# Optimization experiments

Measured on AMD Instinct MI355X. Metric: run time of the kernel, lower is better.

## Reference

```python
import jax, jax.numpy as jnp
import numpy as np

FP8_MAX = 448.0  # float8_e4m3fn max representable magnitude


def _fp8_quant_dequant(x, axis=-1):
    # Per-token (last-axis) dynamic scaling to e4m3, then dequantize back.
    scale = jnp.max(jnp.abs(x), axis=axis, keepdims=True) / FP8_MAX
    scale = jnp.maximum(scale, 1e-12)
    q = (x / scale).astype(jnp.float8_e4m3fn).astype(jnp.float32)
    return q * scale


def setup_inputs() -> dict:
    key = jax.random.key(0)
    k1, k2, k3, k4 = jax.random.split(key, 4)
    S, H, D, T = 64, 64, 128, 32768
    index_q = jax.random.normal(k1, (S, H, D), dtype=jnp.float32)
    index_k = jax.random.normal(k2, (T, D), dtype=jnp.float32)
    weights = jax.random.uniform(k3, (S, H), dtype=jnp.float32)
    cu_seqlen_ks = jnp.zeros((S,), dtype=jnp.int32)
    cu_seqlen_ke = jax.random.randint(k4, (S,), 1, T + 1, dtype=jnp.int32)
    return {
        "index_q": index_q,
        "index_k": index_k,
        "weights": weights,
        "cu_seqlen_ks": cu_seqlen_ks,
        "cu_seqlen_ke": cu_seqlen_ke,
    }


def reference(index_q, index_k, weights, cu_seqlen_ks, cu_seqlen_ke):
    # FP8 (e4m3) quantize-dequantize with per-token dynamic scales.
    q = _fp8_quant_dequant(index_q, axis=-1)   # [S, H, D]
    k = _fp8_quant_dequant(index_k, axis=-1)   # [T, D]
    # Index scores: relu(q.k) weighted-summed over heads -> [S, T]
    scores = jax.nn.relu(jnp.einsum("shd,td->sht", q, k))
    logits = jnp.einsum("sht,sh->st", scores, weights)
    # Ragged KV masking: query s sees kv tokens in [ks[s], ke[s]).
    t = jnp.arange(k.shape[0], dtype=jnp.int32)
    mask = (t[None, :] >= cu_seqlen_ks[:, None]) & (t[None, :] < cu_seqlen_ke[:, None])
    return jnp.where(mask, logits, -jnp.inf)
```

## Files before the change

### kernel.cpp

```cpp
#include <hip/hip_runtime.h>
#include <stdint.h>
#include <math.h>

#define NS 64
#define NH 64
#define ND 128
#define NT 32768
#define CH 1024

#define MASK_VAL (-3.0e38f)

typedef __attribute__((ext_vector_type(4))) float f32x4;

__device__ __align__(16) uint8_t g_q8[NS * NH * ND];
__device__ __align__(16) uint8_t g_k8[NT * ND];
__device__ __align__(16) float g_wq[NS * NH];
__device__ __align__(16) float g_sk[NT];

__device__ __forceinline__ uint32_t f32_to_e4m3(float x) {
  uint32_t u = __float_as_uint(x);
  uint32_t sign = (u >> 24) & 0x80u;
  uint32_t a = u & 0x7FFFFFFFu;
  if (a > 0x43E00000u) a = 0x43E00000u;
  uint32_t e = a >> 23;
  uint32_t code;
  if (e >= 121u) {
    uint32_t m = a & 0x7FFFFFu;
    m += 0x7FFFFu + ((m >> 20) & 1u);
    uint32_t carry = m >> 23;
    code = ((e - 120u + carry) << 3) | (carry ? 0u : ((m >> 20) & 7u));
    if (code > 0x7Eu) code = 0x7Eu;
  } else {
    code = (uint32_t)(int)rintf(__uint_as_float(a) * 512.0f);
  }
  return sign | code;
}

__device__ __forceinline__ void quant_frag(
    const float* __restrict__ in, uint8_t* __restrict__ q8out,
    float* __restrict__ scale_out, const float* __restrict__ wmul,
    int row, int o) {
  const float4* rp = reinterpret_cast<const float4*>(in) + (size_t)row * 32;
  float4 v0 = rp[o * 2];
  float4 v1 = rp[o * 2 + 1];
  float m = fmaxf(fmaxf(fmaxf(fabsf(v0.x), fabsf(v0.y)),
                        fmaxf(fabsf(v0.z), fabsf(v0.w))),
                  fmaxf(fmaxf(fabsf(v1.x), fabsf(v1.y)),
                        fmaxf(fabsf(v1.z), fabsf(v1.w))));
#pragma unroll
  for (int off = 8; off >= 1; off >>= 1)
    m = fmaxf(m, __shfl_xor(m, off, 64));
  float scale = fmaxf(m / 448.0f, 1e-12f);
  uint64_t q = 0;
  q |= (uint64_t)f32_to_e4m3(v0.x / scale);
  q |= (uint64_t)f32_to_e4m3(v0.y / scale) << 8;
  q |= (uint64_t)f32_to_e4m3(v0.z / scale) << 16;
  q |= (uint64_t)f32_to_e4m3(v0.w / scale) << 24;
  q |= (uint64_t)f32_to_e4m3(v1.x / scale) << 32;
  q |= (uint64_t)f32_to_e4m3(v1.y / scale) << 40;
  q |= (uint64_t)f32_to_e4m3(v1.z / scale) << 48;
  q |= (uint64_t)f32_to_e4m3(v1.w / scale) << 56;
  *reinterpret_cast<uint64_t*>(
      q8out + ((size_t)(row >> 4)) * 2048 + o * 128 + (row & 15) * 8) = q;
  if (o == 0) scale_out[row] = wmul ? wmul[row] * scale : scale;
}

__global__ __launch_bounds__(256) void quant_q_kernel(
    const float* __restrict__ in, const float* __restrict__ weights) {
  int w = threadIdx.x >> 6, l = threadIdx.x & 63;
  quant_frag(in, g_q8, g_wq, weights,
             blockIdx.x * 16 + w * 4 + (l >> 4), l & 15);
}

__global__ __launch_bounds__(256) void quant_k_kernel(
    const float* __restrict__ in) {
  int w = threadIdx.x >> 6, l = threadIdx.x & 63;
  quant_frag(in, g_k8, g_sk, nullptr,
             blockIdx.x * 16 + w * 4 + (l >> 4), l & 15);
}

__global__ __launch_bounds__(256) void indexer_main_kernel(
    const int* __restrict__ ksA, const int* __restrict__ keA,
    float* __restrict__ out) {
  const int s = blockIdx.x;
  const int c0 = blockIdx.y * CH;
  const int ks = ksA[s], ke = keA[s];
  const int tid = threadIdx.x;
  float* orow = out + (size_t)s * NT;

  if (c0 >= ke || c0 + CH <= ks) {
#pragma unroll
    for (int i = 0; i < CH / 256; ++i)
      orow[c0 + i * 256 + tid] = MASK_VAL;
    return;
  }

  const int l = tid & 63;
  const int w = tid >> 6;
  const int col = l & 15;
  const int g = l >> 4;

  long a[4][4];
#pragma unroll
  for (int kc = 0; kc < 4; ++kc)
#pragma unroll
    for (int ht = 0; ht < 4; ++ht)
      a[kc][ht] = *reinterpret_cast<const long*>(
          g_q8 + ((size_t)(s * 4 + ht)) * 2048 + kc * 512 + l * 8);

  float4 wq4[4];
#pragma unroll
  for (int ht = 0; ht < 4; ++ht)
    wq4[ht] = *reinterpret_cast<const float4*>(g_wq + s * NH + ht * 16 + g * 4);

#pragma unroll
  for (int i = 0; i < CH / 256; ++i) {
    const int t0w = c0 + i * 256 + w * 64;
    const int t = t0w + l;
    if (t0w >= ke || t0w + 64 <= ks) {
      orow[t] = MASK_VAL;
      continue;
    }

    f32x4 acc[4][4];
    const f32x4 z = {0.f, 0.f, 0.f, 0.f};
#pragma unroll
    for (int x = 0; x < 4; ++x)
#pragma unroll
      for (int y = 0; y < 4; ++y) acc[x][y] = z;

    const uint8_t* kbase = g_k8 + ((size_t)(t0w >> 4)) * 2048;
#pragma unroll
    for (int kc = 0; kc < 4; ++kc) {
      long b[4];
#pragma unroll
      for (int tt = 0; tt < 4; ++tt)
        b[tt] = *reinterpret_cast<const long*>(
            kbase + tt * 2048 + kc * 512 + l * 8);
#pragma unroll
      for (int ht = 0; ht < 4; ++ht)
#pragma unroll
        for (int tt = 0; tt < 4; ++tt)
          acc[ht][tt] = __builtin_amdgcn_mfma_f32_16x16x32_fp8_fp8(
              a[kc][ht], b[tt], acc[ht][tt], 0, 0, 0);
    }

    float r[4];
#pragma unroll
    for (int tt = 0; tt < 4; ++tt) {
      float p = 0.f;
#pragma unroll
      for (int ht = 0; ht < 4; ++ht) {
        p += wq4[ht].x * fmaxf(acc[ht][tt][0], 0.f);
        p += wq4[ht].y * fmaxf(acc[ht][tt][1], 0.f);
        p += wq4[ht].z * fmaxf(acc[ht][tt][2], 0.f);
        p += wq4[ht].w * fmaxf(acc[ht][tt][3], 0.f);
      }
      p += __shfl_xor(p, 16, 64);
      p += __shfl_xor(p, 32, 64);
      r[tt] = p;
    }
    float val = (g == 0) ? r[0] : (g == 1) ? r[1] : (g == 2) ? r[2] : r[3];
    val *= g_sk[t];
    if (((__float_as_uint(val) >> 23) & 0xFFu) == 0xFFu) val = 0.0f;
    orow[t] = (t >= ks && t < ke) ? val : MASK_VAL;
  }
}

extern "C" void kernel_launch(void* const* d_in, const int* in_sizes, int n_in,
                              void* d_out, int out_size, void* d_ws, size_t ws_size,
                              hipStream_t stream) {
  (void)in_sizes; (void)n_in; (void)out_size; (void)d_ws; (void)ws_size;
  const float* index_q = (const float*)d_in[0];
  const float* index_k = (const float*)d_in[1];
  const float* weights = (const float*)d_in[2];
  const int* ksA = (const int*)d_in[3];
  const int* keA = (const int*)d_in[4];
  float* out = (float*)d_out;

  quant_q_kernel<<<dim3((NS * NH) / 16), 256, 0, stream>>>(index_q, weights);
  quant_k_kernel<<<dim3(NT / 16), 256, 0, stream>>>(index_k);
  indexer_main_kernel<<<dim3(NS, NT / CH), 256, 0, stream>>>(ksA, keA, out);
}
```

Measured before the change: 48.83 us.

## Double-buffer K fragment loads across strips and raise occupancy hint

The main kernel now loads each strip's full set of K fragments into one of two register buffers ahead of time, prefetching the next strip while the MFMAs of the current strip run. The aim is to hide global-load latency that was previously exposed before each strip's MFMA chain. Launch bounds also request at least two blocks per CU, which caps register use, while the extra buffered registers add pressure and could cause spills. Prefetch loads are issued even for strips that end up masked, which adds some wasted bandwidth.

```diff
diff --git a/kernel.cpp b/kernel.cpp
--- a/kernel.cpp
+++ b/kernel.cpp
@@ -79,7 +79,60 @@
              blockIdx.x * 16 + w * 4 + (l >> 4), l & 15);
 }
 
-__global__ __launch_bounds__(256) void indexer_main_kernel(
+#define LOADB(BUF, I) do {                                                  \
+    const uint8_t* kb_ = g_k8 + (size_t)(c0 + (I) * 256 + w * 64) * 128;    \
+    _Pragma("unroll")                                                       \
+    for (int kc_ = 0; kc_ < 4; ++kc_)                                       \
+      _Pragma("unroll")                                                     \
+      for (int tt_ = 0; tt_ < 4; ++tt_)                                     \
+        BUF[kc_][tt_] = *reinterpret_cast<const long*>(                     \
+            kb_ + tt_ * 2048 + kc_ * 512 + l * 8);                          \
+  } while (0)
+
+#define STRIP(BUF, I) do {                                                  \
+    const int t0w_ = c0 + (I) * 256 + w * 64;                               \
+    const int t_ = t0w_ + l;                                                \
+    if (t0w_ >= ke || t0w_ + 64 <= ks) {                                    \
+      orow[t_] = MASK_VAL;                                                  \
+    } else {                                                                \
+      f32x4 acc[4][4];                                                      \
+      const f32x4 z_ = {0.f, 0.f, 0.f, 0.f};                                \
+      _Pragma("unroll")                                                     \
+      for (int x_ = 0; x_ < 4; ++x_)                                        \
+        _Pragma("unroll")                                                   \
+        for (int y_ = 0; y_ < 4; ++y_) acc[x_][y_] = z_;                    \
+      _Pragma("unroll")                                                     \
+      for (int kc_ = 0; kc_ < 4; ++kc_)                                     \
+        _Pragma("unroll")                                                   \
+        for (int ht_ = 0; ht_ < 4; ++ht_)                                   \
+          _Pragma("unroll")                                                 \
+          for (int tt_ = 0; tt_ < 4; ++tt_)                                 \
+            acc[ht_][tt_] = __builtin_amdgcn_mfma_f32_16x16x32_fp8_fp8(     \
+                a[kc_][ht_], BUF[kc_][tt_], acc[ht_][tt_], 0, 0, 0);        \
+      float r_[4];                                                          \
+      _Pragma("unroll")                                                     \
+      for (int tt_ = 0; tt_ < 4; ++tt_) {                                   \
+        float p_ = 0.f;                                                     \
+        _Pragma("unroll")                                                   \
+        for (int ht_ = 0; ht_ < 4; ++ht_) {                                 \
+          p_ += wq4[ht_].x * fmaxf(acc[ht_][tt_][0], 0.f);                  \
+          p_ += wq4[ht_].y * fmaxf(acc[ht_][tt_][1], 0.f);                  \
+          p_ += wq4[ht_].z * fmaxf(acc[ht_][tt_][2], 0.f);                  \
+          p_ += wq4[ht_].w * fmaxf(acc[ht_][tt_][3], 0.f);                  \
+        }                                                                   \
+        p_ += __shfl_xor(p_, 16, 64);                                       \
+        p_ += __shfl_xor(p_, 32, 64);                                       \
+        r_[tt_] = p_;                                                       \
+      }                                                                     \
+      float val_ = (g == 0) ? r_[0] : (g == 1) ? r_[1]                      \
+                 : (g == 2) ? r_[2] : r_[3];                                \
+      val_ *= g_sk[t_];                                                     \
+      if (((__float_as_uint(val_) >> 23) & 0xFFu) == 0xFFu) val_ = 0.0f;    \
+      orow[t_] = (t_ >= ks && t_ < ke) ? val_ : MASK_VAL;                   \
+    }                                                                       \
+  } while (0)
+
+__global__ __launch_bounds__(256, 2) void indexer_main_kernel(
     const int* __restrict__ ksA, const int* __restrict__ keA,
     float* __restrict__ out) {
   const int s = blockIdx.x;
@@ -99,6 +152,7 @@
   const int w = tid >> 6;
   const int col = l & 15;
   const int g = l >> 4;
+  (void)col;
 
   long a[4][4];
 #pragma unroll
@@ -113,58 +167,15 @@
   for (int ht = 0; ht < 4; ++ht)
     wq4[ht] = *reinterpret_cast<const float4*>(g_wq + s * NH + ht * 16 + g * 4);
 
-#pragma unroll
-  for (int i = 0; i < CH / 256; ++i) {
-    const int t0w = c0 + i * 256 + w * 64;
-    const int t = t0w + l;
-    if (t0w >= ke || t0w + 64 <= ks) {
-      orow[t] = MASK_VAL;
-      continue;
-    }
-
-    f32x4 acc[4][4];
-    const f32x4 z = {0.f, 0.f, 0.f, 0.f};
-#pragma unroll
-    for (int x = 0; x < 4; ++x)
-#pragma unroll
-      for (int y = 0; y < 4; ++y) acc[x][y] = z;
-
-    const uint8_t* kbase = g_k8 + ((size_t)(t0w >> 4)) * 2048;
-#pragma unroll
-    for (int kc = 0; kc < 4; ++kc) {
-      long b[4];
-#pragma unroll
-      for (int tt = 0; tt < 4; ++tt)
-        b[tt] = *reinterpret_cast<const long*>(
-            kbase + tt * 2048 + kc * 512 + l * 8);
-#pragma unroll
-      for (int ht = 0; ht < 4; ++ht)
-#pragma unroll
-        for (int tt = 0; tt < 4; ++tt)
-          acc[ht][tt] = __builtin_amdgcn_mfma_f32_16x16x32_fp8_fp8(
-              a[kc][ht], b[tt], acc[ht][tt], 0, 0, 0);
-    }
-
-    float r[4];
-#pragma unroll
-    for (int tt = 0; tt < 4; ++tt) {
-      float p = 0.f;
-#pragma unroll
-      for (int ht = 0; ht < 4; ++ht) {
-        p += wq4[ht].x * fmaxf(acc[ht][tt][0], 0.f);
-        p += wq4[ht].y * fmaxf(acc[ht][tt][1], 0.f);
-        p += wq4[ht].z * fmaxf(acc[ht][tt][2], 0.f);
-        p += wq4[ht].w * fmaxf(acc[ht][tt][3], 0.f);
-      }
-      p += __shfl_xor(p, 16, 64);
-      p += __shfl_xor(p, 32, 64);
-      r[tt] = p;
-    }
-    float val = (g == 0) ? r[0] : (g == 1) ? r[1] : (g == 2) ? r[2] : r[3];
-    val *= g_sk[t];
-    if (((__float_as_uint(val) >> 23) & 0xFFu) == 0xFFu) val = 0.0f;
-    orow[t] = (t >= ks && t < ke) ? val : MASK_VAL;
-  }
+  long bP[4][4], bQ[4][4];
+  LOADB(bP, 0);
+  LOADB(bQ, 1);
+  STRIP(bP, 0);
+  LOADB(bP, 2);
+  STRIP(bQ, 1);
+  LOADB(bQ, 3);
+  STRIP(bP, 2);
+  STRIP(bQ, 3);
 }
 
 extern "C" void kernel_launch(void* const* d_in, const int* in_sizes, int n_in,
```

After: 48.05 us. No clear change (-1.6%).

## Pair ke-sorted queries per block to reuse K fragments across two rows

Applied to the files above, without the earlier changes.

Adds a tiny kernel that sorts query rows by their ke end index, then has each main-kernel block process two adjacent sorted queries for one 1024-token chunk. The block loads the K fp8 fragments once and reuses them for both queries' MFMA passes. This halves K reads and gives paired rows similar masking extents, so fewer warps idle. The cost is an extra kernel launch, a dependency on the sort, higher register pressure with both Q fragment sets, and launch bounds of 2 blocks per CU.

```diff
diff --git a/kernel.cpp b/kernel.cpp
--- a/kernel.cpp
+++ b/kernel.cpp
@@ -7,6 +7,8 @@
 #define ND 128
 #define NT 32768
 #define CH 1024
+#define NCH (NT / CH)
+#define SB 2
 
 #define MASK_VAL (-3.0e38f)
 
@@ -16,6 +18,7 @@
 __device__ __align__(16) uint8_t g_k8[NT * ND];
 __device__ __align__(16) float g_wq[NS * NH];
 __device__ __align__(16) float g_sk[NT];
+__device__ int g_perm[NS];
 
 __device__ __forceinline__ uint32_t f32_to_e4m3(float x) {
   uint32_t u = __float_as_uint(x);
@@ -79,91 +82,127 @@
              blockIdx.x * 16 + w * 4 + (l >> 4), l & 15);
 }
 
-__global__ __launch_bounds__(256) void indexer_main_kernel(
+__global__ void sort_ke_kernel(const int* __restrict__ keA) {
+  int l = threadIdx.x;
+  int ke = keA[l];
+  int rank = 0;
+#pragma unroll
+  for (int o = 0; o < NS; ++o) {
+    int keo = __shfl(ke, o, 64);
+    rank += (keo > ke) || (keo == ke && o < l);
+  }
+  g_perm[rank] = l;
+}
+
+__global__ __launch_bounds__(256, 2) void indexer_main_kernel(
     const int* __restrict__ ksA, const int* __restrict__ keA,
     float* __restrict__ out) {
-  const int s = blockIdx.x;
-  const int c0 = blockIdx.y * CH;
-  const int ks = ksA[s], ke = keA[s];
+  const int c0 = blockIdx.x * CH;
+  const int sg = blockIdx.y;
   const int tid = threadIdx.x;
-  float* orow = out + (size_t)s * NT;
-
-  if (c0 >= ke || c0 + CH <= ks) {
-#pragma unroll
-    for (int i = 0; i < CH / 256; ++i)
-      orow[c0 + i * 256 + tid] = MASK_VAL;
-    return;
-  }
-
   const int l = tid & 63;
   const int w = tid >> 6;
-  const int col = l & 15;
   const int g = l >> 4;
 
-  long a[4][4];
+  const int s0 = g_perm[sg * 2], s1 = g_perm[sg * 2 + 1];
+  const int ks0 = ksA[s0], ke0 = keA[s0];
+  const int ks1 = ksA[s1], ke1 = keA[s1];
+  float* orow0 = out + (size_t)s0 * NT;
+  float* orow1 = out + (size_t)s1 * NT;
+
+  const bool act0 = (c0 < ke0) && (c0 + CH > ks0);
+  const bool act1 = (c0 < ke1) && (c0 + CH > ks1);
+  if (!act0 && !act1) {
+#pragma unroll
+    for (int i = 0; i < CH / 256; ++i) {
+      orow0[c0 + i * 256 + tid] = MASK_VAL;
+      orow1[c0 + i * 256 + tid] = MASK_VAL;
+    }
+    return;
+  }
+
+  long a0[4][4], a1[4][4];
 #pragma unroll
   for (int kc = 0; kc < 4; ++kc)
 #pragma unroll
-    for (int ht = 0; ht < 4; ++ht)
-      a[kc][ht] = *reinterpret_cast<const long*>(
-          g_q8 + ((size_t)(s * 4 + ht)) * 2048 + kc * 512 + l * 8);
-
-  float4 wq4[4];
-#pragma unroll
-  for (int ht = 0; ht < 4; ++ht)
-    wq4[ht] = *reinterpret_cast<const float4*>(g_wq + s * NH + ht * 16 + g * 4);
-
-#pragma unroll
-  for (int i = 0; i < CH / 256; ++i) {
+    for (int ht = 0; ht < 4; ++ht) {
+      a0[kc][ht] = *reinterpret_cast<const long*>(
+          g_q8 + ((size_t)(s0 * 4 + ht)) * 2048 + kc * 512 + l * 8);
+      a1[kc][ht] = *reinterpret_cast<const long*>(
+          g_q8 + ((size_t)(s1 * 4 + ht)) * 2048 + kc * 512 + l * 8);
+    }
+  float4 w0[4], w1[4];
+#pragma unroll
+  for (int ht = 0; ht < 4; ++ht) {
+    w0[ht] = *reinterpret_cast<const float4*>(g_wq + s0 * NH + ht * 16 + g * 4);
+    w1[ht] = *reinterpret_cast<const float4*>(g_wq + s1 * NH + ht * 16 + g * 4);
+  }
+
+#pragma unroll
+  for (int i = 0; i < 4; ++i) {
     const int t0w = c0 + i * 256 + w * 64;
     const int t = t0w + l;
-    if (t0w >= ke || t0w + 64 <= ks) {
-      orow[t] = MASK_VAL;
-      continue;
+    const bool m0 = (t0w >= ke0) || (t0w + 64 <= ks0);
+    const bool m1 = (t0w >= ke1) || (t0w + 64 <= ks1);
+    if (m0) orow0[t] = MASK_VAL;
+    if (m1) orow1[t] = MASK_VAL;
+    if (m0 && m1) continue;
+
+    long b[4][4];
+    const uint8_t* kb = g_k8 + (size_t)t0w * 128;
+#pragma unroll
+    for (int kc = 0; kc < 4; ++kc)
+#pragma unroll
+      for (int tt = 0; tt < 4; ++tt)
+        b[kc][tt] = *reinterpret_cast<const long*>(
+            kb + tt * 2048 + kc * 512 + l * 8);
+
+    const float skv = g_sk[t];
+
+#pragma unroll
+    for (int sp = 0; sp < 2; ++sp) {
+      if (sp == 0 ? m0 : m1) continue;
+      f32x4 acc[4][4];
+      const f32x4 z = {0.f, 0.f, 0.f, 0.f};
+#pragma unroll
+      for (int x = 0; x < 4; ++x)
+#pragma unroll
+        for (int y = 0; y < 4; ++y) acc[x][y] = z;
+
+#pragma unroll
+      for (int kc = 0; kc < 4; ++kc)
+#pragma unroll
+        for (int ht = 0; ht < 4; ++ht)
+#pragma unroll
+          for (int tt = 0; tt < 4; ++tt)
+            acc[ht][tt] = __builtin_amdgcn_mfma_f32_16x16x32_fp8_fp8(
+                sp == 0 ? a0[kc][ht] : a1[kc][ht], b[kc][tt],
+                acc[ht][tt], 0, 0, 0);
+
+      float r[4];
+#pragma unroll
+      for (int tt = 0; tt < 4; ++tt) {
+        float p = 0.f;
+#pragma unroll
+        for (int ht = 0; ht < 4; ++ht) {
+          const float4 wq = sp == 0 ? w0[ht] : w1[ht];
+          p += wq.x * fmaxf(acc[ht][tt][0], 0.f);
+          p += wq.y * fmaxf(acc[ht][tt][1], 0.f);
+          p += wq.z * fmaxf(acc[ht][tt][2], 0.f);
+          p += wq.w * fmaxf(acc[ht][tt][3], 0.f);
+        }
+        p += __shfl_xor(p, 16, 64);
+        p += __shfl_xor(p, 32, 64);
+        r[tt] = p;
+      }
+      float val = (g == 0) ? r[0] : (g == 1) ? r[1] : (g == 2) ? r[2] : r[3];
+      val *= skv;
+      if (((__float_as_uint(val) >> 23) & 0xFFu) == 0xFFu) val = 0.0f;
+      const int ks_ = sp == 0 ? ks0 : ks1;
+      const int ke_ = sp == 0 ? ke0 : ke1;
+      float* orow = sp == 0 ? orow0 : orow1;
+      orow[t] = (t >= ks_ && t < ke_) ? val : MASK_VAL;
     }
-
-    f32x4 acc[4][4];
-    const f32x4 z = {0.f, 0.f, 0.f, 0.f};
-#pragma unroll
-    for (int x = 0; x < 4; ++x)
-#pragma unroll
-      for (int y = 0; y < 4; ++y) acc[x][y] = z;
-
-    const uint8_t* kbase = g_k8 + ((size_t)(t0w >> 4)) * 2048;
-#pragma unroll
-    for (int kc = 0; kc < 4; ++kc) {
-      long b[4];
-#pragma unroll
-      for (int tt = 0; tt < 4; ++tt)
-        b[tt] = *reinterpret_cast<const long*>(
-            kbase + tt * 2048 + kc * 512 + l * 8);
-#pragma unroll
-      for (int ht = 0; ht < 4; ++ht)
-#pragma unroll
-        for (int tt = 0; tt < 4; ++tt)
-          acc[ht][tt] = __builtin_amdgcn_mfma_f32_16x16x32_fp8_fp8(
-              a[kc][ht], b[tt], acc[ht][tt], 0, 0, 0);
-    }
-
-    float r[4];
-#pragma unroll
-    for (int tt = 0; tt < 4; ++tt) {
-      float p = 0.f;
-#pragma unroll
-      for (int ht = 0; ht < 4; ++ht) {
-        p += wq4[ht].x * fmaxf(acc[ht][tt][0], 0.f);
-        p += wq4[ht].y * fmaxf(acc[ht][tt][1], 0.f);
-        p += wq4[ht].z * fmaxf(acc[ht][tt][2], 0.f);
-        p += wq4[ht].w * fmaxf(acc[ht][tt][3], 0.f);
-      }
-      p += __shfl_xor(p, 16, 64);
-      p += __shfl_xor(p, 32, 64);
-      r[tt] = p;
-    }
-    float val = (g == 0) ? r[0] : (g == 1) ? r[1] : (g == 2) ? r[2] : r[3];
-    val *= g_sk[t];
-    if (((__float_as_uint(val) >> 23) & 0xFFu) == 0xFFu) val = 0.0f;
-    orow[t] = (t >= ks && t < ke) ? val : MASK_VAL;
   }
 }
 
@@ -180,5 +219,6 @@
 
   quant_q_kernel<<<dim3((NS * NH) / 16), 256, 0, stream>>>(index_q, weights);
   quant_k_kernel<<<dim3(NT / 16), 256, 0, stream>>>(index_k);
-  indexer_main_kernel<<<dim3(NS, NT / CH), 256, 0, stream>>>(ksA, keA, out);
-}
+  sort_ke_kernel<<<dim3(1), 64, 0, stream>>>(keA);
+  indexer_main_kernel<<<dim3(NCH, NS / SB), 256, 0, stream>>>(ksA, keA, out);
+}
```

Result: no change. 48.50 us (-0.7%).
